# Performance work log

Measured on AMD Instinct MI355X. Metric: run time of the kernel, lower is better.

The kernel has to match this reference:

```python
import math
import jax, jax.numpy as jnp
import numpy as np

D_MODEL = 768
NUM_HEADS = 12
NUM_KV_HEADS = 12
FEATURE_DIM = 16
HEAD_DIM = D_MODEL // NUM_KV_HEADS  # 64
EPS = 1e-12
R2 = math.sqrt(2.0)
RD = math.sqrt(FEATURE_DIM)      # sqrt(d)
RRD = math.sqrt(RD)              # d**0.25


def taylor_exp(x):
    """2nd-order Taylor feature map. x: [b,h,l,f] -> [b,h,l,1+f+f^2]."""
    b, h, l, f = x.shape
    x2 = (x[..., :, None] * x[..., None, :]).reshape(b, h, l, f * f) / R2
    ones = jnp.ones((b, h, l, 1), dtype=x.dtype)
    return jnp.concatenate([ones, x / RRD, x2 / RD], axis=-1)


def setup_inputs() -> dict:
    key = jax.random.key(0)
    k0, k1, k2, k3, k4 = jax.random.split(key, 5)
    B, L = 1, 512
    hidden_states = jax.random.normal(k0, (B, L, D_MODEL), dtype=jnp.float32)
    s = 0.02
    Wq = jax.random.normal(k1, (FEATURE_DIM * NUM_HEADS, D_MODEL), dtype=jnp.float32) * s
    Wk = jax.random.normal(k2, (FEATURE_DIM * NUM_KV_HEADS, D_MODEL), dtype=jnp.float32) * s
    Wv = jax.random.normal(k3, (NUM_KV_HEADS * HEAD_DIM, D_MODEL), dtype=jnp.float32) * s
    Wo = jax.random.normal(k4, (D_MODEL, NUM_HEADS * HEAD_DIM), dtype=jnp.float32) * s
    return {"hidden_states": hidden_states, "Wq": Wq, "Wk": Wk, "Wv": Wv, "Wo": Wo}


def reference(hidden_states, Wq, Wk, Wv, Wo):
    b, l, _ = hidden_states.shape
    # projections (nn.Linear, no bias): x @ W.T
    q = (hidden_states @ Wq.T).reshape(b, l, NUM_HEADS, FEATURE_DIM).transpose(0, 2, 1, 3)
    k = (hidden_states @ Wk.T).reshape(b, l, NUM_KV_HEADS, FEATURE_DIM).transpose(0, 2, 1, 3)
    v = (hidden_states @ Wv.T).reshape(b, l, NUM_KV_HEADS, HEAD_DIM).transpose(0, 2, 1, 3)
    q = taylor_exp(q)  # [b,h,l,D], D = 273
    k = taylor_exp(k)
    # causal linear attention: state S_t = sum_{s<=t} v_s phi(k_s)^T
    kv = k[..., None, :] * v[..., :, None]          # [b,h,l,d,D]
    kv = jnp.cumsum(kv, axis=2)
    num = jnp.einsum('bhlD,bhldD->bhld', q, kv)     # [b,h,l,d]
    den = jnp.einsum('bhlD,bhlD->bhl', q, jnp.cumsum(k, axis=2)) + EPS
    y = num / den[..., None]
    y = y.transpose(0, 2, 1, 3).reshape(b, l, NUM_HEADS * HEAD_DIM)
    return y @ Wo.T
```

## Files before the change

kernel.cpp:

```cpp
#include <hip/hip_runtime.h>

typedef short bf16x8 __attribute__((ext_vector_type(8)));
typedef float f32x4 __attribute__((ext_vector_type(4)));

__device__ __forceinline__ unsigned short f2bf(float f) {
  union { float f; unsigned int u; } v; v.f = f;
  unsigned int r = v.u + 0x7FFFu + ((v.u >> 16) & 1u);
  return (unsigned short)(r >> 16);
}

__global__ __launch_bounds__(256) void prep(
    const float* __restrict__ hs, const float* __restrict__ Wq,
    const float* __restrict__ Wk, const float* __restrict__ Wv,
    const float* __restrict__ Wo, unsigned short* __restrict__ hsb,
    unsigned short* __restrict__ Wqkvb, unsigned short* __restrict__ Wob,
    float* __restrict__ numAcc) {
  int b = blockIdx.x;
  const float* src; unsigned short* dst; int base;
  if (b < 384)       { src = hs; dst = hsb;            base = b * 1024; }
  else if (b < 528)  { src = Wq; dst = Wqkvb;          base = (b - 384) * 1024; }
  else if (b < 672)  { src = Wk; dst = Wqkvb + 147456; base = (b - 528) * 1024; }
  else if (b < 1248) { src = Wv; dst = Wqkvb + 294912; base = (b - 672) * 1024; }
  else if (b < 1824) { src = Wo; dst = Wob;            base = (b - 1248) * 1024; }
  else {
    int i = (b - 1824) * 256 + threadIdx.x;
    ((float4*)numAcc)[i] = make_float4(0.f, 0.f, 0.f, 0.f);
    return;
  }
  int i = base + threadIdx.x * 4;
  float4 x = *(const float4*)&src[i];
  ushort4 o;
  o.x = f2bf(x.x); o.y = f2bf(x.y); o.z = f2bf(x.z); o.w = f2bf(x.w);
  *(ushort4*)&dst[i] = o;
}

__global__ __launch_bounds__(256) void gemm_qkv(
    const unsigned short* __restrict__ A, const unsigned short* __restrict__ B,
    unsigned short* __restrict__ C, int N, int K) {
  __shared__ f32x4 part[4][64];
  const int tid = threadIdx.x;
  const int w = tid >> 6, lane = tid & 63;
  const int lm = lane & 15, quad = lane >> 4;
  const int mt = blockIdx.y * 16;
  const int nt = blockIdx.x * 16;
  const int kw = w * (K >> 2);
  const unsigned short* a_ptr = A + (mt + lm) * K + kw + quad * 8;
  const unsigned short* b_ptr = B + (nt + lm) * K + kw + quad * 8;
  f32x4 acc = {0.f, 0.f, 0.f, 0.f};
#pragma unroll
  for (int kb = 0; kb < 192; kb += 32) {
    bf16x8 av = *(const bf16x8*)(a_ptr + kb);
    bf16x8 bv = *(const bf16x8*)(b_ptr + kb);
    acc = __builtin_amdgcn_mfma_f32_16x16x32_bf16(av, bv, acc, 0, 0, 0);
  }
  part[w][lane] = acc;
  __syncthreads();
  if (w == 0) {
    f32x4 s = part[0][lane] + part[1][lane] + part[2][lane] + part[3][lane];
#pragma unroll
    for (int r = 0; r < 4; ++r)
      C[(mt + quad * 4 + r) * N + nt + lm] = f2bf(s[r]);
  }
}

__global__ __launch_bounds__(256) void attn_mfma(
    const unsigned short* __restrict__ QKVb, float* __restrict__ numAcc,
    float* __restrict__ denAcc) {
  int p = blockIdx.x;
  const int h = blockIdx.y, tid = threadIdx.x;
  int c = 0;
  while (p >= c + 1) { p -= c + 1; ++c; }
  const int sb = p;
  const int t0 = c * 64, s0 = sb * 64;
  __shared__ __align__(16) unsigned short Vt[64 * 72];
  __shared__ __align__(16) unsigned short scl[64 * 72];
  __shared__ float denb[64];
  const int w = tid >> 6, lane = tid & 63;
  const int lm = lane & 15, quad = lane >> 4;
#pragma unroll
  for (int pp = 0; pp < 2; ++pp) {
    int idx = pp * 256 + tid;
    int s = idx >> 3, c8 = (idx & 7) * 8;
    bf16x8 v = *(const bf16x8*)&QKVb[(s0 + s) * 1152 + 384 + h * 64 + c8];
#pragma unroll
    for (int j = 0; j < 8; ++j) Vt[(c8 + j) * 72 + s] = ((unsigned short*)&v)[j];
  }
  bf16x8 aq = {0, 0, 0, 0, 0, 0, 0, 0};
  if (quad < 2)
    aq = *(const bf16x8*)&QKVb[(t0 + w * 16 + lm) * 1152 + h * 16 + quad * 8];
  f32x4 qk[4];
#pragma unroll
  for (int sbt = 0; sbt < 4; ++sbt) {
    bf16x8 bk = {0, 0, 0, 0, 0, 0, 0, 0};
    if (quad < 2)
      bk = *(const bf16x8*)&QKVb[(s0 + sbt * 16 + lm) * 1152 + 192 + h * 16 + quad * 8];
    f32x4 z = {0.f, 0.f, 0.f, 0.f};
    qk[sbt] = __builtin_amdgcn_mfma_f32_16x16x32_bf16(aq, bk, z, 0, 0, 0);
  }
  float dsum[4] = {0.f, 0.f, 0.f, 0.f};
#pragma unroll
  for (int sbt = 0; sbt < 4; ++sbt) {
#pragma unroll
    for (int r = 0; r < 4; ++r) {
      int tl = w * 16 + quad * 4 + r;
      int sl = sbt * 16 + lm;
      float x = qk[sbt][r];
      float val = (s0 + sl <= t0 + tl) ? 1.f + 0.25f * x + 0.03125f * x * x : 0.f;
      dsum[r] += val;
      scl[tl * 72 + sl] = f2bf(val);
    }
  }
#pragma unroll
  for (int r = 0; r < 4; ++r) {
    float v = dsum[r];
    v += __shfl_xor(v, 1); v += __shfl_xor(v, 2);
    v += __shfl_xor(v, 4); v += __shfl_xor(v, 8);
    if (lm == 0) denb[w * 16 + quad * 4 + r] = v;
  }
  __syncthreads();
  f32x4 av[4] = {{0.f,0.f,0.f,0.f},{0.f,0.f,0.f,0.f},{0.f,0.f,0.f,0.f},{0.f,0.f,0.f,0.f}};
#pragma unroll
  for (int kb = 0; kb < 2; ++kb) {
    bf16x8 a = *(const bf16x8*)&scl[(w * 16 + lm) * 72 + kb * 32 + quad * 8];
#pragma unroll
    for (int dt = 0; dt < 4; ++dt) {
      bf16x8 b = *(const bf16x8*)&Vt[(dt * 16 + lm) * 72 + kb * 32 + quad * 8];
      av[dt] = __builtin_amdgcn_mfma_f32_16x16x32_bf16(a, b, av[dt], 0, 0, 0);
    }
  }
  if (tid < 64) atomicAdd(&denAcc[(t0 + tid) * 12 + h], denb[tid]);
#pragma unroll
  for (int dt = 0; dt < 4; ++dt)
#pragma unroll
    for (int r = 0; r < 4; ++r)
      atomicAdd(&numAcc[(t0 + w * 16 + quad * 4 + r) * 768 + h * 64 + dt * 16 + lm],
                av[dt][r]);
}

__global__ __launch_bounds__(256) void gemm_out(
    const float* __restrict__ numAcc, const float* __restrict__ denAcc,
    const unsigned short* __restrict__ B, float* __restrict__ out) {
  __shared__ f32x4 part[4][64];
  const int tid = threadIdx.x;
  const int w = tid >> 6, lane = tid & 63;
  const int lm = lane & 15, quad = lane >> 4;
  const int mt = blockIdx.y * 16;
  const int nt = blockIdx.x * 16;
  const int t = mt + lm;
  const int kw = w * 192;
  f32x4 acc = {0.f, 0.f, 0.f, 0.f};
#pragma unroll
  for (int kb = 0; kb < 192; kb += 32) {
    int k0 = kw + kb + quad * 8;
    float inv = 1.f / (denAcc[t * 12 + (k0 >> 6)] + 1e-12f);
    float4 n0 = *(const float4*)&numAcc[t * 768 + k0];
    float4 n1 = *(const float4*)&numAcc[t * 768 + k0 + 4];
    bf16x8 a;
    a[0] = f2bf(n0.x * inv); a[1] = f2bf(n0.y * inv);
    a[2] = f2bf(n0.z * inv); a[3] = f2bf(n0.w * inv);
    a[4] = f2bf(n1.x * inv); a[5] = f2bf(n1.y * inv);
    a[6] = f2bf(n1.z * inv); a[7] = f2bf(n1.w * inv);
    bf16x8 bv = *(const bf16x8*)&B[(nt + lm) * 768 + k0];
    acc = __builtin_amdgcn_mfma_f32_16x16x32_bf16(a, bv, acc, 0, 0, 0);
  }
  part[w][lane] = acc;
  __syncthreads();
  if (w == 0) {
    f32x4 s = part[0][lane] + part[1][lane] + part[2][lane] + part[3][lane];
#pragma unroll
    for (int r = 0; r < 4; ++r)
      out[(mt + quad * 4 + r) * 768 + nt + lm] = s[r];
  }
}

extern "C" void kernel_launch(void* const* d_in, const int* in_sizes, int n_in,
                              void* d_out, int out_size, void* d_ws, size_t ws_size,
                              hipStream_t stream) {
  const float* hs = (const float*)d_in[0];
  const float* Wq = (const float*)d_in[1];
  const float* Wk = (const float*)d_in[2];
  const float* Wv = (const float*)d_in[3];
  const float* Wo = (const float*)d_in[4];
  float* out = (float*)d_out;
  float* ws = (float*)d_ws;

  float* numAcc = ws;
  float* denAcc = ws + 393216;
  unsigned short* hsb   = (unsigned short*)(ws + 399360);
  unsigned short* Wqkvb = hsb + 393216;
  unsigned short* Wob   = Wqkvb + 884736;
  unsigned short* QKVb  = Wob + 589824;

  prep<<<dim3(2214), 256, 0, stream>>>(hs, Wq, Wk, Wv, Wo, hsb, Wqkvb, Wob, numAcc);
  gemm_qkv<<<dim3(72, 32), 256, 0, stream>>>(hsb, Wqkvb, QKVb, 1152, 768);
  attn_mfma<<<dim3(36, 12), 256, 0, stream>>>(QKVb, numAcc, denAcc);
  gemm_out<<<dim3(48, 32), 256, 0, stream>>>(numAcc, denAcc, Wob, out);
}
```

Measured before the change: 109.3 us.

## Fuse bf16 conversion into GEMMs and replace attention atomics with split partial sums

Removes the separate prep kernel by converting fp32 inputs and weights to bf16 inside the QKV and output GEMMs. The QKV GEMM now writes V already transposed, so attention no longer builds a transposed V tile in shared memory. Attention loops over key blocks inside each block, with the work split across two halves, and writes plain partial sums instead of issuing atomicAdds. The output GEMM then adds the two partials. This drops one launch, the zeroing pass and the atomic traffic, but weights are re-converted in every tile, and a per-block causal loop can leave the load unbalanced.

New measurement: 135.3 us. +23.8%, slower.

```diff
diff --git a/kernel.cpp b/kernel.cpp
--- a/kernel.cpp
+++ b/kernel.cpp
@@ -9,105 +9,102 @@
   return (unsigned short)(r >> 16);
 }
 
-__global__ __launch_bounds__(256) void prep(
-    const float* __restrict__ hs, const float* __restrict__ Wq,
-    const float* __restrict__ Wk, const float* __restrict__ Wv,
-    const float* __restrict__ Wo, unsigned short* __restrict__ hsb,
-    unsigned short* __restrict__ Wqkvb, unsigned short* __restrict__ Wob,
-    float* __restrict__ numAcc) {
-  int b = blockIdx.x;
-  const float* src; unsigned short* dst; int base;
-  if (b < 384)       { src = hs; dst = hsb;            base = b * 1024; }
-  else if (b < 528)  { src = Wq; dst = Wqkvb;          base = (b - 384) * 1024; }
-  else if (b < 672)  { src = Wk; dst = Wqkvb + 147456; base = (b - 528) * 1024; }
-  else if (b < 1248) { src = Wv; dst = Wqkvb + 294912; base = (b - 672) * 1024; }
-  else if (b < 1824) { src = Wo; dst = Wob;            base = (b - 1248) * 1024; }
-  else {
-    int i = (b - 1824) * 256 + threadIdx.x;
-    ((float4*)numAcc)[i] = make_float4(0.f, 0.f, 0.f, 0.f);
-    return;
-  }
-  int i = base + threadIdx.x * 4;
-  float4 x = *(const float4*)&src[i];
-  ushort4 o;
-  o.x = f2bf(x.x); o.y = f2bf(x.y); o.z = f2bf(x.z); o.w = f2bf(x.w);
-  *(ushort4*)&dst[i] = o;
+__device__ __forceinline__ bf16x8 cvt8(const float* __restrict__ p) {
+  float4 a = *(const float4*)p;
+  float4 b = *(const float4*)(p + 4);
+  bf16x8 r;
+  r[0] = f2bf(a.x); r[1] = f2bf(a.y); r[2] = f2bf(a.z); r[3] = f2bf(a.w);
+  r[4] = f2bf(b.x); r[5] = f2bf(b.y); r[6] = f2bf(b.z); r[7] = f2bf(b.w);
+  return r;
 }
 
 __global__ __launch_bounds__(256) void gemm_qkv(
-    const unsigned short* __restrict__ A, const unsigned short* __restrict__ B,
-    unsigned short* __restrict__ C, int N, int K) {
+    const float* __restrict__ hs, const float* __restrict__ Wq,
+    const float* __restrict__ Wk, const float* __restrict__ Wv,
+    unsigned short* __restrict__ QKb, unsigned short* __restrict__ Vt) {
   __shared__ f32x4 part[4][64];
   const int tid = threadIdx.x;
   const int w = tid >> 6, lane = tid & 63;
   const int lm = lane & 15, quad = lane >> 4;
   const int mt = blockIdx.y * 16;
-  const int nt = blockIdx.x * 16;
-  const int kw = w * (K >> 2);
-  const unsigned short* a_ptr = A + (mt + lm) * K + kw + quad * 8;
-  const unsigned short* b_ptr = B + (nt + lm) * K + kw + quad * 8;
+  const int n0 = blockIdx.x * 16;
+  const float* B; int bn;
+  if (n0 < 192)      { B = Wq; bn = n0; }
+  else if (n0 < 384) { B = Wk; bn = n0 - 192; }
+  else               { B = Wv; bn = n0 - 384; }
+  const int kw = w * 192;
+  const float* a_ptr = hs + (mt + lm) * 768 + kw + quad * 8;
+  const float* b_ptr = B + (bn + lm) * 768 + kw + quad * 8;
   f32x4 acc = {0.f, 0.f, 0.f, 0.f};
 #pragma unroll
   for (int kb = 0; kb < 192; kb += 32) {
-    bf16x8 av = *(const bf16x8*)(a_ptr + kb);
-    bf16x8 bv = *(const bf16x8*)(b_ptr + kb);
+    bf16x8 av = cvt8(a_ptr + kb);
+    bf16x8 bv = cvt8(b_ptr + kb);
     acc = __builtin_amdgcn_mfma_f32_16x16x32_bf16(av, bv, acc, 0, 0, 0);
   }
   part[w][lane] = acc;
   __syncthreads();
   if (w == 0) {
     f32x4 s = part[0][lane] + part[1][lane] + part[2][lane] + part[3][lane];
+    if (n0 < 384) {
 #pragma unroll
-    for (int r = 0; r < 4; ++r)
-      C[(mt + quad * 4 + r) * N + nt + lm] = f2bf(s[r]);
+      for (int r = 0; r < 4; ++r)
+        QKb[(mt + quad * 4 + r) * 384 + n0 + lm] = f2bf(s[r]);
+    } else {
+      ushort4 o;
+      o.x = f2bf(s[0]); o.y = f2bf(s[1]); o.z = f2bf(s[2]); o.w = f2bf(s[3]);
+      *(ushort4*)&Vt[(n0 - 384 + lm) * 512 + mt + quad * 4] = o;
+    }
   }
 }
 
-__global__ __launch_bounds__(256) void attn_mfma(
-    const unsigned short* __restrict__ QKVb, float* __restrict__ numAcc,
-    float* __restrict__ denAcc) {
-  int p = blockIdx.x;
-  const int h = blockIdx.y, tid = threadIdx.x;
-  int c = 0;
-  while (p >= c + 1) { p -= c + 1; ++c; }
-  const int sb = p;
-  const int t0 = c * 64, s0 = sb * 64;
-  __shared__ __align__(16) unsigned short Vt[64 * 72];
-  __shared__ __align__(16) unsigned short scl[64 * 72];
-  __shared__ float denb[64];
+__global__ __launch_bounds__(256) void attn(
+    const unsigned short* __restrict__ QKb, const unsigned short* __restrict__ Vt,
+    float* __restrict__ numP, float* __restrict__ denP) {
+  const int c = blockIdx.x, h = blockIdx.y, half = blockIdx.z;
+  const int tid = threadIdx.x;
   const int w = tid >> 6, lane = tid & 63;
   const int lm = lane & 15, quad = lane >> 4;
-#pragma unroll
-  for (int pp = 0; pp < 2; ++pp) {
-    int idx = pp * 256 + tid;
-    int s = idx >> 3, c8 = (idx & 7) * 8;
-    bf16x8 v = *(const bf16x8*)&QKVb[(s0 + s) * 1152 + 384 + h * 64 + c8];
-#pragma unroll
-    for (int j = 0; j < 8; ++j) Vt[(c8 + j) * 72 + s] = ((unsigned short*)&v)[j];
-  }
+  __shared__ __align__(16) unsigned short scl[2][64 * 72];
+  const int t0 = c * 64;
   bf16x8 aq = {0, 0, 0, 0, 0, 0, 0, 0};
   if (quad < 2)
-    aq = *(const bf16x8*)&QKVb[(t0 + w * 16 + lm) * 1152 + h * 16 + quad * 8];
-  f32x4 qk[4];
+    aq = *(const bf16x8*)&QKb[(t0 + w * 16 + lm) * 384 + h * 16 + quad * 8];
+  f32x4 av[4] = {{0.f,0.f,0.f,0.f},{0.f,0.f,0.f,0.f},{0.f,0.f,0.f,0.f},{0.f,0.f,0.f,0.f}};
+  float dsum[4] = {0.f, 0.f, 0.f, 0.f};
+  const unsigned short* vbase = Vt + (h * 64 + lm) * 512;
+  for (int sb = half; sb <= c; sb += 2) {
+    const int s0 = sb * 64;
+    f32x4 qk[4];
 #pragma unroll
-  for (int sbt = 0; sbt < 4; ++sbt) {
-    bf16x8 bk = {0, 0, 0, 0, 0, 0, 0, 0};
-    if (quad < 2)
-      bk = *(const bf16x8*)&QKVb[(s0 + sbt * 16 + lm) * 1152 + 192 + h * 16 + quad * 8];
-    f32x4 z = {0.f, 0.f, 0.f, 0.f};
-    qk[sbt] = __builtin_amdgcn_mfma_f32_16x16x32_bf16(aq, bk, z, 0, 0, 0);
-  }
-  float dsum[4] = {0.f, 0.f, 0.f, 0.f};
+    for (int sbt = 0; sbt < 4; ++sbt) {
+      bf16x8 bk = {0, 0, 0, 0, 0, 0, 0, 0};
+      if (quad < 2)
+        bk = *(const bf16x8*)&QKb[(s0 + sbt * 16 + lm) * 384 + 192 + h * 16 + quad * 8];
+      f32x4 z = {0.f, 0.f, 0.f, 0.f};
+      qk[sbt] = __builtin_amdgcn_mfma_f32_16x16x32_bf16(aq, bk, z, 0, 0, 0);
+    }
+    unsigned short* sw = &scl[sb & 1][0];
 #pragma unroll
-  for (int sbt = 0; sbt < 4; ++sbt) {
+    for (int sbt = 0; sbt < 4; ++sbt) {
 #pragma unroll
-    for (int r = 0; r < 4; ++r) {
-      int tl = w * 16 + quad * 4 + r;
-      int sl = sbt * 16 + lm;
-      float x = qk[sbt][r];
-      float val = (s0 + sl <= t0 + tl) ? 1.f + 0.25f * x + 0.03125f * x * x : 0.f;
-      dsum[r] += val;
-      scl[tl * 72 + sl] = f2bf(val);
+      for (int r = 0; r < 4; ++r) {
+        int tl = w * 16 + quad * 4 + r;
+        int sl = sbt * 16 + lm;
+        float x = qk[sbt][r];
+        float val = (s0 + sl <= t0 + tl) ? 1.f + 0.25f * x + 0.03125f * x * x : 0.f;
+        dsum[r] += val;
+        sw[tl * 72 + sl] = f2bf(val);
+      }
+    }
+#pragma unroll
+    for (int kb = 0; kb < 2; ++kb) {
+      bf16x8 a = *(const bf16x8*)&sw[(w * 16 + lm) * 72 + kb * 32 + quad * 8];
+#pragma unroll
+      for (int dt = 0; dt < 4; ++dt) {
+        bf16x8 b = *(const bf16x8*)&vbase[dt * 16 * 512 + s0 + kb * 32 + quad * 8];
+        av[dt] = __builtin_amdgcn_mfma_f32_16x16x32_bf16(a, b, av[dt], 0, 0, 0);
+      }
     }
   }
 #pragma unroll
@@ -115,31 +112,19 @@
     float v = dsum[r];
     v += __shfl_xor(v, 1); v += __shfl_xor(v, 2);
     v += __shfl_xor(v, 4); v += __shfl_xor(v, 8);
-    if (lm == 0) denb[w * 16 + quad * 4 + r] = v;
+    if (lm == 0) denP[half * 6144 + (t0 + w * 16 + quad * 4 + r) * 12 + h] = v;
   }
-  __syncthreads();
-  f32x4 av[4] = {{0.f,0.f,0.f,0.f},{0.f,0.f,0.f,0.f},{0.f,0.f,0.f,0.f},{0.f,0.f,0.f,0.f}};
-#pragma unroll
-  for (int kb = 0; kb < 2; ++kb) {
-    bf16x8 a = *(const bf16x8*)&scl[(w * 16 + lm) * 72 + kb * 32 + quad * 8];
-#pragma unroll
-    for (int dt = 0; dt < 4; ++dt) {
-      bf16x8 b = *(const bf16x8*)&Vt[(dt * 16 + lm) * 72 + kb * 32 + quad * 8];
-      av[dt] = __builtin_amdgcn_mfma_f32_16x16x32_bf16(a, b, av[dt], 0, 0, 0);
-    }
-  }
-  if (tid < 64) atomicAdd(&denAcc[(t0 + tid) * 12 + h], denb[tid]);
+  float* np = numP + half * 393216;
 #pragma unroll
   for (int dt = 0; dt < 4; ++dt)
 #pragma unroll
     for (int r = 0; r < 4; ++r)
-      atomicAdd(&numAcc[(t0 + w * 16 + quad * 4 + r) * 768 + h * 64 + dt * 16 + lm],
-                av[dt][r]);
+      np[(t0 + w * 16 + quad * 4 + r) * 768 + h * 64 + dt * 16 + lm] = av[dt][r];
 }
 
 __global__ __launch_bounds__(256) void gemm_out(
-    const float* __restrict__ numAcc, const float* __restrict__ denAcc,
-    const unsigned short* __restrict__ B, float* __restrict__ out) {
+    const float* __restrict__ numP, const float* __restrict__ denP,
+    const float* __restrict__ Wo, float* __restrict__ out) {
   __shared__ f32x4 part[4][64];
   const int tid = threadIdx.x;
   const int w = tid >> 6, lane = tid & 63;
@@ -152,15 +137,19 @@
 #pragma unroll
   for (int kb = 0; kb < 192; kb += 32) {
     int k0 = kw + kb + quad * 8;
-    float inv = 1.f / (denAcc[t * 12 + (k0 >> 6)] + 1e-12f);
-    float4 n0 = *(const float4*)&numAcc[t * 768 + k0];
-    float4 n1 = *(const float4*)&numAcc[t * 768 + k0 + 4];
+    int hh = k0 >> 6;
+    float den = denP[t * 12 + hh] + denP[6144 + t * 12 + hh] + 1e-12f;
+    float inv = 1.f / den;
+    const float* n0p = numP + t * 768 + k0;
+    const float* n1p = numP + 393216 + t * 768 + k0;
+    float4 x0 = *(const float4*)n0p, x1 = *(const float4*)(n0p + 4);
+    float4 y0 = *(const float4*)n1p, y1 = *(const float4*)(n1p + 4);
     bf16x8 a;
-    a[0] = f2bf(n0.x * inv); a[1] = f2bf(n0.y * inv);
-    a[2] = f2bf(n0.z * inv); a[3] = f2bf(n0.w * inv);
-    a[4] = f2bf(n1.x * inv); a[5] = f2bf(n1.y * inv);
-    a[6] = f2bf(n1.z * inv); a[7] = f2bf(n1.w * inv);
-    bf16x8 bv = *(const bf16x8*)&B[(nt + lm) * 768 + k0];
+    a[0] = f2bf((x0.x + y0.x) * inv); a[1] = f2bf((x0.y + y0.y) * inv);
+    a[2] = f2bf((x0.z + y0.z) * inv); a[3] = f2bf((x0.w + y0.w) * inv);
+    a[4] = f2bf((x1.x + y1.x) * inv); a[5] = f2bf((x1.y + y1.y) * inv);
+    a[6] = f2bf((x1.z + y1.z) * inv); a[7] = f2bf((x1.w + y1.w) * inv);
+    bf16x8 bv = cvt8(Wo + (nt + lm) * 768 + k0);
     acc = __builtin_amdgcn_mfma_f32_16x16x32_bf16(a, bv, acc, 0, 0, 0);
   }
   part[w][lane] = acc;
@@ -184,15 +173,12 @@
   float* out = (float*)d_out;
   float* ws = (float*)d_ws;
 
-  float* numAcc = ws;
-  float* denAcc = ws + 393216;
-  unsigned short* hsb   = (unsigned short*)(ws + 399360);
-  unsigned short* Wqkvb = hsb + 393216;
-  unsigned short* Wob   = Wqkvb + 884736;
-  unsigned short* QKVb  = Wob + 589824;
+  float* numP = ws;
+  float* denP = ws + 786432;
+  unsigned short* QKb = (unsigned short*)(ws + 798720);
+  unsigned short* Vt  = QKb + 196608;
 
-  prep<<<dim3(2214), 256, 0, stream>>>(hs, Wq, Wk, Wv, Wo, hsb, Wqkvb, Wob, numAcc);
-  gemm_qkv<<<dim3(72, 32), 256, 0, stream>>>(hsb, Wqkvb, QKVb, 1152, 768);
-  attn_mfma<<<dim3(36, 12), 256, 0, stream>>>(QKVb, numAcc, denAcc);
-  gemm_out<<<dim3(48, 32), 256, 0, stream>>>(numAcc, denAcc, Wob, out);
+  gemm_qkv<<<dim3(72, 32), 256, 0, stream>>>(hs, Wq, Wk, Wv, QKb, Vt);
+  attn<<<dim3(8, 12, 2), 256, 0, stream>>>(QKb, Vt, numP, denP);
+  gemm_out<<<dim3(48, 32), 256, 0, stream>>>(numP, denP, Wo, out);
 }
```
